# Kernel optimization log

Measured on AMD Instinct MI355X. Metric: run time of the kernel, lower is better.

## Reference

```python
import jax, jax.numpy as jnp
import numpy as np

WIN = (7, 7)
SHIFT = (3, 3)
HEADS = 12


def _rel_index():
    wh, ww = WIN
    coords = np.stack(np.meshgrid(np.arange(wh), np.arange(ww), indexing='ij')).reshape(2, -1)
    rel = (coords[:, :, None] - coords[:, None, :]).transpose(1, 2, 0).astype(np.int64)
    rel[:, :, 0] += wh - 1
    rel[:, :, 1] += ww - 1
    rel[:, :, 0] *= 2 * ww - 1
    return rel.sum(-1).reshape(-1)  # [N*N]


def _attn_mask(pH, pW, sh, sw):
    wh, ww = WIN
    mask = np.zeros((pH, pW), np.float32)
    h_sl = [(0, pH - wh), (pH - wh, pH - sh), (pH - sh, pH)]
    w_sl = [(0, pW - ww), (pW - ww, pW - sw), (pW - sw, pW)]
    cnt = 0
    for hs in h_sl:
        for ws in w_sl:
            mask[hs[0]:hs[1], ws[0]:ws[1]] = cnt
            cnt += 1
    nw = (pH // wh) * (pW // ww)
    mask = mask.reshape(pH // wh, wh, pW // ww, ww).transpose(0, 2, 1, 3).reshape(nw, wh * ww)
    diff = mask[:, None, :] - mask[:, :, None]
    return jnp.asarray(np.where(diff != 0, -100.0, 0.0).astype(np.float32))  # [nw, N, N]


def setup_inputs() -> dict:
    key = jax.random.key(0)
    ks = jax.random.split(key, 6)
    C = 384
    return {
        'x': jax.random.normal(ks[0], (16, 56, 56, C), jnp.float32),
        'qkv_weight': jax.random.normal(ks[1], (3 * C, C), jnp.float32) * 0.02,
        'qkv_bias': jax.random.normal(ks[2], (3 * C,), jnp.float32) * 0.02,
        'proj_weight': jax.random.normal(ks[3], (C, C), jnp.float32) * 0.02,
        'proj_bias': jax.random.normal(ks[4], (C,), jnp.float32) * 0.02,
        'rel_table': jax.random.normal(ks[5], (169, HEADS), jnp.float32) * 0.02,
    }


def reference(x, qkv_weight, qkv_bias, proj_weight, proj_bias, rel_table):
    B, H, W, C = x.shape
    wh, ww = WIN
    pad_b = (wh - H % wh) % wh
    pad_r = (ww - W % ww) % ww
    xp = jnp.pad(x, ((0, 0), (0, pad_b), (0, pad_r), (0, 0)))
    pH, pW = H + pad_b, W + pad_r
    sh = 0 if wh >= pH else SHIFT[0]
    sw = 0 if ww >= pW else SHIFT[1]
    shifted = (sh + sw) > 0
    if shifted:
        xp = jnp.roll(xp, (-sh, -sw), axis=(1, 2))
    nwh, nww = pH // wh, pW // ww
    nw, N = nwh * nww, wh * ww
    # window partition -> [B*nw, N, C]
    xw = xp.reshape(B, nwh, wh, nww, ww, C).transpose(0, 1, 3, 2, 4, 5).reshape(B * nw, N, C)
    qkv = xw @ qkv_weight.T + qkv_bias
    qkv = qkv.reshape(B * nw, N, 3, HEADS, C // HEADS).transpose(2, 0, 3, 1, 4)
    q, k, v = qkv[0], qkv[1], qkv[2]  # [B*nw, heads, N, hd]
    q = q * (C // HEADS) ** -0.5
    attn = jnp.einsum('whnd,whmd->whnm', q, k)
    bias = rel_table[jnp.asarray(_rel_index())].reshape(N, N, HEADS).transpose(2, 0, 1)
    attn = attn + bias[None]
    if shifted:
        mask = _attn_mask(pH, pW, sh, sw)  # [nw, N, N]
        attn = (attn.reshape(B, nw, HEADS, N, N) + mask[None, :, None]).reshape(B * nw, HEADS, N, N)
    attn = jax.nn.softmax(attn, axis=-1)
    out = jnp.einsum('whnm,whmd->whnd', attn, v).transpose(0, 2, 1, 3).reshape(B * nw, N, C)
    out = out @ proj_weight.T + proj_bias
    out = out.reshape(B, nwh, nww, wh, ww, C).transpose(0, 1, 3, 2, 4, 5).reshape(B, pH, pW, C)
    if shifted:
        out = jnp.roll(out, (sh, sw), axis=(1, 2))
    return out[:, :H, :W, :]
```

## Files before the change

kernel.cpp:

```cpp
#include <hip/hip_runtime.h>

#define CCH 384
#define NHEADS 12
#define HDIM 32
#define NTOK 49
#define NWIN 1024
#define MROWS 50176
#define PSTR 72

typedef __attribute__((ext_vector_type(8))) short bf16x8;
typedef __attribute__((ext_vector_type(4))) float f32x4;

#define WAITVM_BAR(N) asm volatile("s_waitcnt vmcnt(" #N ")\n\ts_barrier" ::: "memory")
#define BAR() asm volatile("s_barrier" ::: "memory")

__device__ __forceinline__ unsigned short f2bf(float f) {
    unsigned u = __builtin_bit_cast(unsigned, f);
    u += 0x7FFFu + ((u >> 16) & 1u);
    return (unsigned short)(u >> 16);
}

__device__ __forceinline__ void g2lds16(const unsigned short* g, unsigned short* l) {
    __builtin_amdgcn_global_load_lds(
        (const __attribute__((address_space(1))) unsigned int*)g,
        (__attribute__((address_space(3))) unsigned int*)l,
        16, 0, 0);
}

__device__ __forceinline__ size_t row_to_pixel(int r) {
    int wlin = r / 49, n = r - wlin * 49;
    int b = wlin >> 6, wimg = wlin & 63;
    int wy = wimg >> 3, wx = wimg & 7;
    int iy = n / 7, ix = n - iy * 7;
    int y = wy * 7 + iy + 3; if (y >= 56) y -= 56;
    int x = wx * 7 + ix + 3; if (x >= 56) x -= 56;
    return (size_t)((b * 56 + y) * 56 + x);
}

__global__ __launch_bounds__(256) void prep_gather(const float* __restrict__ xin,
                            unsigned short* __restrict__ xw,
                            const float* __restrict__ qkvw, const float* __restrict__ projw,
                            const float* __restrict__ rel_table,
                            unsigned short* __restrict__ wq, unsigned short* __restrict__ wp,
                            float* __restrict__ btt2) {
    const int blk = blockIdx.x;
    if (blk < 18816) {
        int idx = blk * 256 + threadIdx.x;
        int row = idx / 96, c4 = (idx - row * 96) * 4;
        const float4 v = *(const float4*)(xin + row_to_pixel(row) * CCH + c4);
        ushort4 o;
        o.x = f2bf(v.x); o.y = f2bf(v.y); o.z = f2bf(v.z); o.w = f2bf(v.w);
        *(ushort4*)(xw + (size_t)row * CCH + c4) = o;
        return;
    }
    int i = (blk - 18816) * 256 + threadIdx.x;
    if (i < 3 * CCH * CCH) wq[i] = f2bf(qkvw[i]);
    if (i < CCH * CCH) wp[i] = f2bf(projw[i]);
    if (i < 4 * NHEADS * 16 * 64) {
        int cls = i / (NHEADS * 16 * 64);
        int rem = i - cls * (NHEADS * 16 * 64);
        int h = rem / (16 * 64);
        int rem2 = rem - h * (16 * 64);
        int rb = rem2 >> 6, cj = rem2 & 63;
        int jreg = 0;
        if (cj < NTOK) {
            int jy = cj / 7, jx = cj - jy * 7;
            int ry = (cls & 2) ? ((jy < 4) ? 1 : 2) : 0;
            int rx = (cls & 1) ? ((jx < 4) ? 1 : 2) : 0;
            jreg = ry * 3 + rx;
        }
        float4 o;
        float* po = (float*)&o;
#pragma unroll
        for (int rr = 0; rr < 4; ++rr) {
            int ri = rb * 4 + rr;
            float v = -1e30f;
            if (ri < NTOK && cj < NTOK) {
                int iy = ri / 7, ix = ri - iy * 7;
                int jy = cj / 7, jx = cj - jy * 7;
                int idx = (iy - jy + 6) * 13 + (ix - jx + 6);
                v = rel_table[idx * NHEADS + h];
                int ry = (cls & 2) ? ((iy < 4) ? 1 : 2) : 0;
                int rx = (cls & 1) ? ((ix < 4) ? 1 : 2) : 0;
                if (ry * 3 + rx != jreg) v -= 100.f;
            }
            po[rr] = v;
        }
        *(float4*)&btt2[(size_t)i * 4] = o;
    }
}

__global__ __launch_bounds__(512) void qkv_gemm(const unsigned short* __restrict__ xw,
        const unsigned short* __restrict__ wq, const float* __restrict__ qkv_bias,
        unsigned short* __restrict__ qb, unsigned short* __restrict__ kb,
        unsigned short* __restrict__ vb) {
    __shared__ unsigned short As[2][256 * 32];
    __shared__ unsigned short Bs[2][128 * 32];
    const int tid = threadIdx.x;
    const int bid = blockIdx.x;
    const int xcd = bid & 7;
    const int base = (xcd < 4) ? xcd * 221 : (4 * 221 + (xcd - 4) * 220);
    const int swz = base + (bid >> 3);
    const int rb = swz / 9, cb = swz - rb * 9;
    const int row0 = rb * 256;
    const int col0 = cb * 128;
    const int lane = tid & 63, wv = tid >> 6;
    const int wm = wv >> 1, wn = wv & 1;
    const int l15 = lane & 15, g = lane >> 4;

    const int lrow = lane >> 2;
    const int lc = lane & 3;
    const int scs = ((lc ^ ((lrow >> 1) & 3)) * 8);
    const unsigned short* gA0 = xw + (size_t)(row0 + wv * 32 + lrow) * CCH + scs;
    const unsigned short* gA1 = gA0 + (size_t)16 * CCH;
    const unsigned short* gB0 = wq + (size_t)(col0 + wv * 16 + lrow) * CCH + scs;
    const int rc = (g ^ ((l15 >> 1) & 3)) * 8;

    f32x4 acc[4][4];
#pragma unroll
    for (int i = 0; i < 4; ++i)
#pragma unroll
        for (int j = 0; j < 4; ++j) acc[i][j] = (f32x4){0.f, 0.f, 0.f, 0.f};

    g2lds16(gA0, &As[0][wv * 1024]);
    g2lds16(gA1, &As[0][wv * 1024 + 512]);
    g2lds16(gB0, &Bs[0][wv * 512]);
    WAITVM_BAR(0);

#pragma unroll
    for (int kk = 0; kk < 12; ++kk) {
        const int cur = kk & 1;
        if (kk < 11) {
            const int nxt = cur ^ 1;
            g2lds16(gA0 + (kk + 1) * 32, &As[nxt][wv * 1024]);
            g2lds16(gA1 + (kk + 1) * 32, &As[nxt][wv * 1024 + 512]);
            g2lds16(gB0 + (kk + 1) * 32, &Bs[nxt][wv * 512]);
        }
        bf16x8 af[4], bfv[4];
#pragma unroll
        for (int mt = 0; mt < 4; ++mt)
            af[mt] = *(const bf16x8*)&As[cur][(wm * 64 + mt * 16 + l15) * 32 + rc];
#pragma unroll
        for (int nt = 0; nt < 4; ++nt)
            bfv[nt] = *(const bf16x8*)&Bs[cur][(wn * 64 + nt * 16 + l15) * 32 + rc];
#pragma unroll
        for (int mt = 0; mt < 4; ++mt)
#pragma unroll
            for (int nt = 0; nt < 4; ++nt)
                acc[mt][nt] = __builtin_amdgcn_mfma_f32_16x16x32_bf16(af[mt], bfv[nt], acc[mt][nt], 0, 0, 0);
        if (kk < 11) WAITVM_BAR(0);
    }

    const float SCALE = 0.17677669529663687f;
#pragma unroll
    for (int nt = 0; nt < 4; ++nt) {
        int col = col0 + wn * 64 + nt * 16 + l15;
        float bias = qkv_bias[col];
        int which = col / CCH;
        int rem = col - which * CCH;
        int h = rem >> 5, d = rem & 31;
        unsigned short* dstb = (which == 0) ? qb : ((which == 1) ? kb : vb);
        float scl = (which == 0) ? SCALE : 1.0f;
#pragma unroll
        for (int mt = 0; mt < 4; ++mt) {
#pragma unroll
            for (int rr = 0; rr < 4; ++rr) {
                int row = row0 + wm * 64 + mt * 16 + g * 4 + rr;
                int w2 = row / 49, n2 = row - w2 * 49;
                size_t inst = (size_t)(w2 * NHEADS + h);
                float v = (acc[mt][nt][rr] + bias) * scl;
                dstb[(inst * NTOK + n2) * HDIM + d] = f2bf(v);
            }
        }
    }
}

__global__ __launch_bounds__(256) void attn_kernel(const unsigned short* __restrict__ qbuf,
        const unsigned short* __restrict__ kbuf, const unsigned short* __restrict__ vbuf,
        const float* __restrict__ btt2, unsigned short* __restrict__ ao) {
    __shared__ unsigned short Ps[4][64 * PSTR];
    __shared__ unsigned short Vt[4][32 * 64];
    const int tid = threadIdx.x;
    const int lane = tid & 63, wv = tid >> 6;
    const int inst = blockIdx.x * 4 + wv;
    const int w = inst / NHEADS, h = inst - w * NHEADS;
    const int l15 = lane & 15, g = lane >> 4;
    const unsigned short* qp = qbuf + (size_t)inst * (NTOK * HDIM);
    const unsigned short* kp = kbuf + (size_t)inst * (NTOK * HDIM);
    const unsigned short* vp = vbuf + (size_t)inst * (NTOK * HDIM);

    const bf16x8 zero8 = {0, 0, 0, 0, 0, 0, 0, 0};
    bf16x8 vpre[4];
#pragma unroll
    for (int p = 0; p < 4; ++p) {
        int e0 = (p * 64 + lane) * 8;
        int tok = e0 >> 5;
        vpre[p] = (tok < NTOK) ? *(const bf16x8*)&vp[e0] : zero8;
    }

    bf16x8 aq[4], bk[4];
#pragma unroll
    for (int mt = 0; mt < 4; ++mt) {
        int row = mt * 16 + l15;
        aq[mt] = (row < NTOK) ? *(const bf16x8*)&qp[row * HDIM + g * 8] : zero8;
    }
#pragma unroll
    for (int nt = 0; nt < 4; ++nt) {
        int colk = nt * 16 + l15;
        bk[nt] = (colk < NTOK) ? *(const bf16x8*)&kp[colk * HDIM + g * 8] : zero8;
    }
    f32x4 s[4][4];
#pragma unroll
    for (int mt = 0; mt < 4; ++mt)
#pragma unroll
        for (int nt = 0; nt < 4; ++nt)
            s[mt][nt] = __builtin_amdgcn_mfma_f32_16x16x32_bf16(aq[mt], bk[nt], (f32x4){0.f, 0.f, 0.f, 0.f}, 0, 0, 0);

    {
        unsigned short* vt = Vt[wv];
#pragma unroll
        for (int p = 0; p < 4; ++p) {
            int e0 = (p * 64 + lane) * 8;
            int tok = e0 >> 5, d0 = e0 & 31;
#pragma unroll
            for (int j = 0; j < 8; ++j) {
                int d = d0 + j;
                vt[d * 64 + (tok ^ ((d & 7) << 3))] = (unsigned short)vpre[p][j];
            }
        }
    }

    const int wimg = w & 63;
    const int wy = wimg >> 3, wx = wimg & 7;
    const int wcls = (((wy == 7) ? 2 : 0) | ((wx == 7) ? 1 : 0));
    const float4* bt4 = (const float4*)btt2 + ((size_t)(wcls * NHEADS + h)) * (16 * 64);

    float inv[4][4];
#pragma unroll
    for (int mt = 0; mt < 4; ++mt) {
        float4 bias4[4];
#pragma unroll
        for (int nt = 0; nt < 4; ++nt)
            bias4[nt] = bt4[(mt * 4 + g) * 64 + nt * 16 + l15];
#pragma unroll
        for (int rr = 0; rr < 4; ++rr) {
#pragma unroll
            for (int nt = 0; nt < 4; ++nt) {
                float bb = (rr == 0) ? bias4[nt].x : (rr == 1) ? bias4[nt].y : (rr == 2) ? bias4[nt].z : bias4[nt].w;
                s[mt][nt][rr] += bb;
            }
            float m = fmaxf(fmaxf(s[mt][0][rr], s[mt][1][rr]), fmaxf(s[mt][2][rr], s[mt][3][rr]));
            m = fmaxf(m, __shfl_xor(m, 1));
            m = fmaxf(m, __shfl_xor(m, 2));
            m = fmaxf(m, __shfl_xor(m, 4));
            m = fmaxf(m, __shfl_xor(m, 8));
            float sum = 0.f;
#pragma unroll
            for (int nt = 0; nt < 4; ++nt) {
                float p = __expf(s[mt][nt][rr] - m);
                s[mt][nt][rr] = p;
                sum += p;
            }
            sum += __shfl_xor(sum, 1);
            sum += __shfl_xor(sum, 2);
            sum += __shfl_xor(sum, 4);
            sum += __shfl_xor(sum, 8);
            inv[mt][rr] = 1.0f / sum;
        }
    }
    unsigned short* ps = Ps[wv];
#pragma unroll
    for (int mt = 0; mt < 4; ++mt)
#pragma unroll
        for (int nt = 0; nt < 4; ++nt)
#pragma unroll
            for (int rr = 0; rr < 4; ++rr)
                ps[(mt * 16 + g * 4 + rr) * PSTR + nt * 16 + l15] = f2bf(s[mt][nt][rr]);

    f32x4 o[4][2];
#pragma unroll
    for (int mt = 0; mt < 4; ++mt)
#pragma unroll
        for (int dt = 0; dt < 2; ++dt) o[mt][dt] = (f32x4){0.f, 0.f, 0.f, 0.f};

    const unsigned short* vt = Vt[wv];
#pragma unroll
    for (int kt = 0; kt < 2; ++kt) {
        bf16x8 ap[4];
#pragma unroll
        for (int mt = 0; mt < 4; ++mt)
            ap[mt] = *(const bf16x8*)&ps[(mt * 16 + l15) * PSTR + kt * 32 + g * 8];
#pragma unroll
        for (int dt = 0; dt < 2; ++dt) {
            const int d = dt * 16 + l15;
            const int cb = kt * 32 + g * 8;
            bf16x8 bv = *(const bf16x8*)&vt[d * 64 + (cb ^ ((d & 7) << 3))];
#pragma unroll
            for (int mt = 0; mt < 4; ++mt)
                o[mt][dt] = __builtin_amdgcn_mfma_f32_16x16x32_bf16(ap[mt], bv, o[mt][dt], 0, 0, 0);
        }
    }
#pragma unroll
    for (int mt = 0; mt < 4; ++mt)
#pragma unroll
        for (int dt = 0; dt < 2; ++dt)
#pragma unroll
            for (int rr = 0; rr < 4; ++rr) {
                int row = mt * 16 + g * 4 + rr;
                if (row < NTOK) {
                    float val = o[mt][dt][rr] * inv[mt][rr];
                    ao[((size_t)(w * NTOK + row)) * CCH + h * HDIM + dt * 16 + l15] = f2bf(val);
                }
            }
}

__global__ __launch_bounds__(256) void proj_gemm(const unsigned short* __restrict__ ain,
        const unsigned short* __restrict__ wp, const float* __restrict__ proj_bias,
        float* __restrict__ out) {
    __shared__ unsigned short As[2][128 * 32];
    __shared__ unsigned short Bs[2][128 * 32];
    const int tid = threadIdx.x;
    const int bid = blockIdx.x;
    const int swz = (bid & 7) * 147 + (bid >> 3);
    const int rbk = swz / 3, cbk = swz - rbk * 3;
    const int row0 = rbk * 128;
    const int col0 = cbk * 128;
    const int lane = tid & 63, wv = tid >> 6;
    const int wm = wv >> 1, wn = wv & 1;
    const int l15 = lane & 15, g = lane >> 4;

    const int srow = wv * 16 + (lane >> 2);
    const int scs = (((lane & 3) ^ ((srow >> 1) & 3)) * 8);
    const unsigned short* gA0 = ain + (size_t)(row0 + srow) * CCH + scs;
    const unsigned short* gA1 = gA0 + (size_t)64 * CCH;
    const unsigned short* gB0 = wp + (size_t)(col0 + srow) * CCH + scs;
    const unsigned short* gB1 = gB0 + (size_t)64 * CCH;
    const int rc = (g ^ ((l15 >> 1) & 3)) * 8;

    f32x4 acc[4][4];
#pragma unroll
    for (int i = 0; i < 4; ++i)
#pragma unroll
        for (int j = 0; j < 4; ++j) acc[i][j] = (f32x4){0.f, 0.f, 0.f, 0.f};

    g2lds16(gA0, &As[0][wv * 512]);
    g2lds16(gA1, &As[0][wv * 512 + 2048]);
    g2lds16(gB0, &Bs[0][wv * 512]);
    g2lds16(gB1, &Bs[0][wv * 512 + 2048]);
    WAITVM_BAR(0);

#pragma unroll
    for (int kk = 0; kk < 12; ++kk) {
        const int cur = kk & 1;
        if (kk < 11) {
            const int nxt = cur ^ 1;
            g2lds16(gA0 + (kk + 1) * 32, &As[nxt][wv * 512]);
            g2lds16(gA1 + (kk + 1) * 32, &As[nxt][wv * 512 + 2048]);
            g2lds16(gB0 + (kk + 1) * 32, &Bs[nxt][wv * 512]);
            g2lds16(gB1 + (kk + 1) * 32, &Bs[nxt][wv * 512 + 2048]);
        }
        bf16x8 af[4], bfv[4];
#pragma unroll
        for (int mt = 0; mt < 4; ++mt)
            af[mt] = *(const bf16x8*)&As[cur][(wm * 64 + mt * 16 + l15) * 32 + rc];
#pragma unroll
        for (int nt = 0; nt < 4; ++nt)
            bfv[nt] = *(const bf16x8*)&Bs[cur][(wn * 64 + nt * 16 + l15) * 32 + rc];
#pragma unroll
        for (int mt = 0; mt < 4; ++mt)
#pragma unroll
            for (int nt = 0; nt < 4; ++nt)
                acc[mt][nt] = __builtin_amdgcn_mfma_f32_16x16x32_bf16(af[mt], bfv[nt], acc[mt][nt], 0, 0, 0);
        if (kk < 11) WAITVM_BAR(0);
    }
#pragma unroll
    for (int nt = 0; nt < 4; ++nt) {
        int col = col0 + wn * 64 + nt * 16 + l15;
        float bias = proj_bias[col];
#pragma unroll
        for (int mt = 0; mt < 4; ++mt) {
#pragma unroll
            for (int rr = 0; rr < 4; ++rr) {
                int row = row0 + wm * 64 + mt * 16 + g * 4 + rr;
                out[row_to_pixel(row) * CCH + col] = acc[mt][nt][rr] + bias;
            }
        }
    }
}

extern "C" void kernel_launch(void* const* d_in, const int* in_sizes, int n_in,
                              void* d_out, int out_size, void* d_ws, size_t ws_size,
                              hipStream_t stream) {
    const float* x     = (const float*)d_in[0];
    const float* qkvw  = (const float*)d_in[1];
    const float* qkvb  = (const float*)d_in[2];
    const float* projw = (const float*)d_in[3];
    const float* projb = (const float*)d_in[4];
    const float* rel   = (const float*)d_in[5];
    float* out = (float*)d_out;

    char* ws = (char*)d_ws;
    unsigned short* wqb = (unsigned short*)(ws);
    unsigned short* wpb = (unsigned short*)(ws + 884736);
    float* btt2         = (float*)(ws + 884736 + 294912);
    const size_t off  = 2097152;
    const size_t bufb = 38535168ull;
    unsigned short* qb  = (unsigned short*)(ws + off);
    unsigned short* kb  = (unsigned short*)(ws + off + bufb);
    unsigned short* vb  = (unsigned short*)(ws + off + 2 * bufb);
    unsigned short* ao  = (unsigned short*)(ws + off + 3 * bufb);
    unsigned short* xw  = ao;

    prep_gather<<<20544, 256, 0, stream>>>(x, xw, qkvw, projw, rel, wqb, wpb, btt2);
    qkv_gemm<<<1764, 512, 0, stream>>>(xw, wqb, qkvb, qb, kb, vb);
    attn_kernel<<<3072, 256, 0, stream>>>(qb, kb, vb, btt2, ao);
    proj_gemm<<<1176, 256, 0, stream>>>(ao, wpb, projb, out);
}
```

Measured before the change: 163.6 us.

## Triple-buffer QKV GEMM loads and widen gather to 8 elements per thread

The QKV GEMM moves from double to triple buffering of its LDS tiles. Loads are issued two k-steps ahead, and each step waits only until the oldest group has landed (vmcnt 3) instead of draining all loads. The gather/convert stage now handles 8 floats per thread with 16-byte bf16 stores, which halves its block count. The GEMM change uses more LDS (72KB per block), which may lower occupancy, and it relies on a single barrier per iteration to protect buffer reuse.

Measured after the change: 168.7 us. 1.03x slower.

```diff
diff --git a/kernel.cpp b/kernel.cpp
--- a/kernel.cpp
+++ b/kernel.cpp
@@ -44,16 +44,21 @@
                             unsigned short* __restrict__ wq, unsigned short* __restrict__ wp,
                             float* __restrict__ btt2) {
     const int blk = blockIdx.x;
-    if (blk < 18816) {
+    if (blk < 9408) {
         int idx = blk * 256 + threadIdx.x;
-        int row = idx / 96, c4 = (idx - row * 96) * 4;
-        const float4 v = *(const float4*)(xin + row_to_pixel(row) * CCH + c4);
-        ushort4 o;
-        o.x = f2bf(v.x); o.y = f2bf(v.y); o.z = f2bf(v.z); o.w = f2bf(v.w);
-        *(ushort4*)(xw + (size_t)row * CCH + c4) = o;
+        int row = idx / 48, cc = (idx - row * 48) * 8;
+        const float* src = xin + row_to_pixel(row) * CCH + cc;
+        const float4 v0 = *(const float4*)(src);
+        const float4 v1 = *(const float4*)(src + 4);
+        bf16x8 o;
+        o[0] = (short)f2bf(v0.x); o[1] = (short)f2bf(v0.y);
+        o[2] = (short)f2bf(v0.z); o[3] = (short)f2bf(v0.w);
+        o[4] = (short)f2bf(v1.x); o[5] = (short)f2bf(v1.y);
+        o[6] = (short)f2bf(v1.z); o[7] = (short)f2bf(v1.w);
+        *(bf16x8*)(xw + (size_t)row * CCH + cc) = o;
         return;
     }
-    int i = (blk - 18816) * 256 + threadIdx.x;
+    int i = (blk - 9408) * 256 + threadIdx.x;
     if (i < 3 * CCH * CCH) wq[i] = f2bf(qkvw[i]);
     if (i < CCH * CCH) wp[i] = f2bf(projw[i]);
     if (i < 4 * NHEADS * 16 * 64) {
@@ -94,8 +99,8 @@
         const unsigned short* __restrict__ wq, const float* __restrict__ qkv_bias,
         unsigned short* __restrict__ qb, unsigned short* __restrict__ kb,
         unsigned short* __restrict__ vb) {
-    __shared__ unsigned short As[2][256 * 32];
-    __shared__ unsigned short Bs[2][128 * 32];
+    __shared__ unsigned short As[3][256 * 32];
+    __shared__ unsigned short Bs[3][128 * 32];
     const int tid = threadIdx.x;
     const int bid = blockIdx.x;
     const int xcd = bid & 7;
@@ -125,16 +130,23 @@
     g2lds16(gA0, &As[0][wv * 1024]);
     g2lds16(gA1, &As[0][wv * 1024 + 512]);
     g2lds16(gB0, &Bs[0][wv * 512]);
-    WAITVM_BAR(0);
+    g2lds16(gA0 + 32, &As[1][wv * 1024]);
+    g2lds16(gA1 + 32, &As[1][wv * 1024 + 512]);
+    g2lds16(gB0 + 32, &Bs[1][wv * 512]);
 
 #pragma unroll
     for (int kk = 0; kk < 12; ++kk) {
-        const int cur = kk & 1;
+        const int cur = kk % 3;
         if (kk < 11) {
-            const int nxt = cur ^ 1;
-            g2lds16(gA0 + (kk + 1) * 32, &As[nxt][wv * 1024]);
-            g2lds16(gA1 + (kk + 1) * 32, &As[nxt][wv * 1024 + 512]);
-            g2lds16(gB0 + (kk + 1) * 32, &Bs[nxt][wv * 512]);
+            WAITVM_BAR(3);
+        } else {
+            WAITVM_BAR(0);
+        }
+        if (kk < 10) {
+            const int nx2 = (kk + 2) % 3;
+            g2lds16(gA0 + (kk + 2) * 32, &As[nx2][wv * 1024]);
+            g2lds16(gA1 + (kk + 2) * 32, &As[nx2][wv * 1024 + 512]);
+            g2lds16(gB0 + (kk + 2) * 32, &Bs[nx2][wv * 512]);
         }
         bf16x8 af[4], bfv[4];
 #pragma unroll
@@ -148,7 +160,6 @@
 #pragma unroll
             for (int nt = 0; nt < 4; ++nt)
                 acc[mt][nt] = __builtin_amdgcn_mfma_f32_16x16x32_bf16(af[mt], bfv[nt], acc[mt][nt], 0, 0, 0);
-        if (kk < 11) WAITVM_BAR(0);
     }
 
     const float SCALE = 0.17677669529663687f;
@@ -411,7 +422,7 @@
     unsigned short* ao  = (unsigned short*)(ws + off + 3 * bufb);
     unsigned short* xw  = ao;
 
-    prep_gather<<<20544, 256, 0, stream>>>(x, xw, qkvw, projw, rel, wqb, wpb, btt2);
+    prep_gather<<<11136, 256, 0, stream>>>(x, xw, qkvw, projw, rel, wqb, wpb, btt2);
     qkv_gemm<<<1764, 512, 0, stream>>>(xw, wqb, qkvb, qb, kb, vb);
     attn_kernel<<<3072, 256, 0, stream>>>(qb, kb, vb, btt2, ao);
     proj_gemm<<<1176, 256, 0, stream>>>(ao, wpb, projb, out);
```
